# Kernel tuning notes

Measured on AMD Instinct MI355X. Metric: run time of the kernel, lower is better.

## Reference

```python
import jax, jax.numpy as jnp
import numpy as np

H = 16  # num_heads

def setup_inputs() -> dict:
    key = jax.random.key(0)
    ks = jax.random.split(key, 9)
    B, S, E = 2, 2048, 1024
    d = E // H  # 64, shared KV head dim
    sc = lambda n: 1.0 / np.sqrt(n)
    return {
        "x": jax.random.normal(ks[0], (B, S, E), jnp.float32),
        "wq": jax.random.normal(ks[1], (E, E), jnp.float32) * sc(E),
        "bq": jax.random.normal(ks[2], (E,), jnp.float32) * 0.02,
        "wk": jax.random.normal(ks[3], (E, d), jnp.float32) * sc(E),
        "bk": jax.random.normal(ks[4], (d,), jnp.float32) * 0.02,
        "wv": jax.random.normal(ks[5], (E, d), jnp.float32) * sc(E),
        "bv": jax.random.normal(ks[6], (d,), jnp.float32) * 0.02,
        "wo": jax.random.normal(ks[7], (E, E), jnp.float32) * sc(E),
        "bo": jax.random.normal(ks[8], (E,), jnp.float32) * 0.02,
    }

def reference(x, wq, bq, wk, bk, wv, bv, wo, bo):
    B, S, E = x.shape
    d = E // H
    Q = (x @ wq + bq).reshape(B, S, H, d).transpose(0, 2, 1, 3)  # [B,H,S,d]
    K = x @ wk + bk  # [B,S,d] shared across heads (MQA)
    V = x @ wv + bv  # [B,S,d]
    scores = jnp.einsum('bhqd,bkd->bhqk', Q, K) / np.sqrt(d)  # [B,H,S,S]
    weights = jax.nn.softmax(scores, axis=-1)
    attn = jnp.einsum('bhqk,bkd->bhqd', weights, V)  # [B,H,S,d]
    # FAITHFUL to source: reshape [B,H,S,d] -> [B,S,E] WITHOUT permuting back
    attn = attn.reshape(B, S, E)
    return attn @ wo + bo
```

## Files before the change

### kernel.cpp

```cpp
#include <hip/hip_runtime.h>
#include <hip/hip_bf16.h>

#define BB 2
#define SS 2048
#define EE 1024
#define HH 16
#define DD 64

using bfrag  = __attribute__((ext_vector_type(8))) short;
using bfrag4 = __attribute__((ext_vector_type(4))) short;
using ffrag  = __attribute__((ext_vector_type(4))) float;
using uint2v = __attribute__((ext_vector_type(2))) uint;

#define MFMA32(A, B, C) __builtin_amdgcn_mfma_f32_16x16x32_bf16(A, B, C, 0, 0, 0)
#define MFMA16(A, B, C) __builtin_amdgcn_mfma_f32_16x16x16bf16_1k(A, B, C, 0, 0, 0)

static __device__ __forceinline__ ushort f2bf(float f) {
  __hip_bfloat16 h = __float2bfloat16(f);
  return *reinterpret_cast<ushort*>(&h);
}

static __device__ __forceinline__ uint pack_bf2(float lo, float hi) {
  uint a = __float_as_uint(lo) + 0x8000u;
  uint b = __float_as_uint(hi) + 0x8000u;
  return __builtin_amdgcn_perm(b, a, 0x07060302u);
}

static __device__ __forceinline__ void gl_lds16(const ushort* g, ushort* l) {
  __builtin_amdgcn_global_load_lds(
      (const __attribute__((address_space(1))) void*)g,
      (__attribute__((address_space(3))) void*)l, 16, 0, 0);
}

__global__ __launch_bounds__(256) void prep(
    const float* __restrict__ x, const float* __restrict__ wq,
    const float* __restrict__ wk, const float* __restrict__ wv,
    const float* __restrict__ wo, ushort* __restrict__ xb,
    ushort* __restrict__ wqkvT, ushort* __restrict__ woT) {
  __shared__ float t[32][33];
  int id = blockIdx.x;
  if (id < 4096) {
    int i = id * 256 + threadIdx.x;
    float4 v = ((const float4*)x)[i];
    ushort4 u = { f2bf(v.x), f2bf(v.y), f2bf(v.z), f2bf(v.w) };
    ((ushort4*)xb)[i] = u;
    return;
  }
  id -= 4096;
  const float* src;
  ushort* dst;
  int N, bx, by;
  if (id < 1024)      { src = wq; dst = wqkvT;                      N = 1024; bx = id & 31;          by = id >> 5; }
  else if (id < 2048) { src = wo; dst = woT;                        N = 1024; bx = (id - 1024) & 31; by = (id - 1024) >> 5; }
  else if (id < 2112) { src = wk; dst = wqkvT + (size_t)1024 * 1024; N = 64;  bx = (id - 2048) & 1;  by = (id - 2048) >> 1; }
  else                { src = wv; dst = wqkvT + (size_t)1088 * 1024; N = 64;  bx = (id - 2112) & 1;  by = (id - 2112) >> 1; }
  const int k0 = by * 32, n0 = bx * 32;
  const int tx = threadIdx.x & 31, ty = threadIdx.x >> 5;
  #pragma unroll
  for (int i = 0; i < 32; i += 8)
    t[ty + i][tx] = src[(size_t)(k0 + ty + i) * N + n0 + tx];
  __syncthreads();
  #pragma unroll
  for (int i = 0; i < 32; i += 8)
    dst[(size_t)(n0 + ty + i) * 1024 + k0 + tx] = f2bf(t[tx][ty + i]);
}

template <bool QKV>
__global__ __launch_bounds__(256) void gemm_mfma3(
    const ushort* __restrict__ A, const ushort* __restrict__ Bt,
    const float* __restrict__ bias0, const float* __restrict__ bias1,
    const float* __restrict__ bias2, void* __restrict__ O1,
    ushort* __restrict__ Kb, ushort* __restrict__ VTb,
    int M, int N, int K, float qscale) {
  __shared__ __align__(16) ushort As[2][128 * 64];
  __shared__ __align__(16) ushort Bs[2][64 * 64];
  const int tid = threadIdx.x;
  const int lane = tid & 63;
  const int quad = lane >> 4;
  const int c = lane & 15;
  const int wv = tid >> 6;
  const int wm = (wv & 1) * 64;
  const int wn = (wv >> 1) * 32;
  const size_t m0 = (size_t)blockIdx.y * 128;
  const size_t n0 = (size_t)blockIdx.x * 64;

  const int srow = lane >> 3;
  const int sck = (lane & 7) ^ srow;

  ffrag zero = {0.f, 0.f, 0.f, 0.f};
  ffrag acc[4][2];
  #pragma unroll
  for (int mt = 0; mt < 4; ++mt)
    #pragma unroll
    for (int nt = 0; nt < 2; ++nt) acc[mt][nt] = zero;

  const int NK = K >> 6;
  #pragma unroll
  for (int i = 0; i < 4; ++i) {
    int ia = wv * 4 + i;
    gl_lds16(&A[(m0 + ia * 8 + srow) * (size_t)K + sck * 8], &As[0][ia * 512]);
  }
  #pragma unroll
  for (int i = 0; i < 2; ++i) {
    int ib = wv * 2 + i;
    gl_lds16(&Bt[(n0 + ib * 8 + srow) * (size_t)K + sck * 8], &Bs[0][ib * 512]);
  }
  __syncthreads();

  for (int ki = 0; ki < NK; ++ki) {
    const int buf = ki & 1;
    if (ki + 1 < NK) {
      int k0 = (ki + 1) << 6;
      #pragma unroll
      for (int i = 0; i < 4; ++i) {
        int ia = wv * 4 + i;
        gl_lds16(&A[(m0 + ia * 8 + srow) * (size_t)K + k0 + sck * 8],
                 &As[buf ^ 1][ia * 512]);
      }
      #pragma unroll
      for (int i = 0; i < 2; ++i) {
        int ib = wv * 2 + i;
        gl_lds16(&Bt[(n0 + ib * 8 + srow) * (size_t)K + k0 + sck * 8],
                 &Bs[buf ^ 1][ib * 512]);
      }
    }
    #pragma unroll
    for (int ks = 0; ks < 2; ++ks) {
      bfrag af[4], bf[2];
      #pragma unroll
      for (int mt = 0; mt < 4; ++mt) {
        int ra = wm + mt * 16 + c;
        af[mt] = *(const bfrag*)&As[buf][(ra * 8 + ((ks * 4 + quad) ^ (ra & 7))) * 8];
      }
      #pragma unroll
      for (int nt = 0; nt < 2; ++nt) {
        int rb = wn + nt * 16 + c;
        bf[nt] = *(const bfrag*)&Bs[buf][(rb * 8 + ((ks * 4 + quad) ^ (rb & 7))) * 8];
      }
      #pragma unroll
      for (int mt = 0; mt < 4; ++mt)
        #pragma unroll
        for (int nt = 0; nt < 2; ++nt)
          acc[mt][nt] = MFMA32(af[mt], bf[nt], acc[mt][nt]);
    }
    __syncthreads();
  }

  #pragma unroll
  for (int nt = 0; nt < 2; ++nt) {
    const int colb = (int)n0 + wn + nt * 16;
    if (QKV) {
      if (colb < 1024) {
        float bb = bias0[colb + c];
        ushort* dst = (ushort*)O1 + colb;
        #pragma unroll
        for (int mt = 0; mt < 4; ++mt)
          #pragma unroll
          for (int r = 0; r < 4; ++r) {
            size_t row = m0 + wm + mt * 16 + quad * 4 + r;
            dst[row * 1024 + c] = f2bf((acc[mt][nt][r] + bb) * qscale);
          }
      } else if (colb < 1088) {
        float bb = bias1[colb - 1024 + c];
        ushort* dst = Kb + (colb - 1024);
        #pragma unroll
        for (int mt = 0; mt < 4; ++mt)
          #pragma unroll
          for (int r = 0; r < 4; ++r) {
            size_t row = m0 + wm + mt * 16 + quad * 4 + r;
            dst[row * 64 + c] = f2bf(acc[mt][nt][r] + bb);
          }
      } else {
        int d = colb - 1088 + c;
        float bb = bias2[colb - 1088 + c];
        int bidx = (int)(m0 >> 11);
        ushort* dstv = VTb + ((size_t)(bidx * 64 + d)) * SS;
        #pragma unroll
        for (int mt = 0; mt < 4; ++mt) {
          int sb = (int)(m0 & 2047) + wm + mt * 16 + quad * 4;
          uint2v u;
          u.x = pack_bf2(acc[mt][nt][0] + bb, acc[mt][nt][1] + bb);
          u.y = pack_bf2(acc[mt][nt][2] + bb, acc[mt][nt][3] + bb);
          *(uint2v*)&dstv[sb] = u;
        }
      }
    } else {
      float bb = bias0[colb + c];
      float* dst = (float*)O1;
      #pragma unroll
      for (int mt = 0; mt < 4; ++mt)
        #pragma unroll
        for (int r = 0; r < 4; ++r) {
          size_t row = m0 + wm + mt * 16 + quad * 4 + r;
          dst[row * (size_t)N + colb + c] = acc[mt][nt][r] + bb;
        }
    }
  }
}

__global__ __launch_bounds__(256) void mqa_attn8(
    const ushort* __restrict__ Q, const ushort* __restrict__ Kg,
    const ushort* __restrict__ VT, ushort* __restrict__ A2) {
  __shared__ __align__(16) ushort Kt[2][4096];
  __shared__ __align__(16) ushort Vt[2][4096];
  const int tid = threadIdx.x;
  const int lane = tid & 63;
  const int quad = lane >> 4;
  const int c = lane & 15;
  const int wv = tid >> 6;
  const int bid = blockIdx.x;
  const int b = bid >> 8;
  const int r = bid & 255;
  const int h = r >> 4;
  const int s0 = (r & 15) << 7;

  const int srow = lane >> 3;
  const int sck = (lane & 7) ^ srow;

  ffrag zero = {0.f, 0.f, 0.f, 0.f};
  bfrag4 ones4;
  #pragma unroll
  for (int i = 0; i < 4; ++i) ones4[i] = (short)16256;

  bfrag aq[2][2];
  #pragma unroll
  for (int mt = 0; mt < 2; ++mt) {
    const ushort* qp =
        Q + ((size_t)(b * SS) + s0 + wv * 32 + mt * 16 + c) * EE + h * 64 + quad * 8;
    aq[mt][0] = *(const bfrag*)qp;
    aq[mt][1] = *(const bfrag*)(qp + 32);
  }

  ffrag o[2][4];
  #pragma unroll
  for (int mt = 0; mt < 2; ++mt)
    #pragma unroll
    for (int nt = 0; nt < 4; ++nt) o[mt][nt] = zero;
  ffrag ls[2] = {zero, zero};

  const ushort* Kbase = Kg + (size_t)b * SS * 64;
  const ushort* Vbase = VT + (size_t)b * 64 * SS;
  const int i0 = wv * 2, i1 = wv * 2 + 1;
  const int r0 = i0 * 8 + srow, r1 = i1 * 8 + srow;

  gl_lds16(Kbase + (size_t)r0 * 64 + sck * 8, &Kt[0][i0 * 512]);
  gl_lds16(Kbase + (size_t)r1 * 64 + sck * 8, &Kt[0][i1 * 512]);
  gl_lds16(Vbase + (size_t)r0 * SS + sck * 8, &Vt[0][i0 * 512]);
  gl_lds16(Vbase + (size_t)r1 * SS + sck * 8, &Vt[0][i1 * 512]);
  __syncthreads();

  for (int it = 0; it < 32; ++it) {
    const int buf = it & 1;
    if (it + 1 < 32) {
      int kb = (it + 1) << 6;
      gl_lds16(Kbase + (size_t)(kb + r0) * 64 + sck * 8, &Kt[buf ^ 1][i0 * 512]);
      gl_lds16(Kbase + (size_t)(kb + r1) * 64 + sck * 8, &Kt[buf ^ 1][i1 * 512]);
      gl_lds16(Vbase + (size_t)r0 * SS + kb + sck * 8, &Vt[buf ^ 1][i0 * 512]);
      gl_lds16(Vbase + (size_t)r1 * SS + kb + sck * 8, &Vt[buf ^ 1][i1 * 512]);
    }

    #pragma unroll
    for (int kt = 0; kt < 4; ++kt) {
      const int key = kt * 16 + c;
      const int k7 = key & 7;
      bfrag kf0 = *(const bfrag*)&Kt[buf][(key * 8 + (quad ^ k7)) * 8];
      bfrag kf1 = *(const bfrag*)&Kt[buf][(key * 8 + ((quad + 4) ^ k7)) * 8];
      bfrag4 pb[2];
      #pragma unroll
      for (int mt = 0; mt < 2; ++mt) {
        ffrag st = MFMA32(kf0, aq[mt][0], zero);
        st = MFMA32(kf1, aq[mt][1], st);
        uint2v uu;
        uu.x = pack_bf2(__builtin_amdgcn_exp2f(st[0]),
                        __builtin_amdgcn_exp2f(st[1]));
        uu.y = pack_bf2(__builtin_amdgcn_exp2f(st[2]),
                        __builtin_amdgcn_exp2f(st[3]));
        pb[mt] = __builtin_bit_cast(bfrag4, uu);
      }
      const int ck = kt * 2 + (quad >> 1);
      const int wc = (quad & 1) * 4;
      #pragma unroll
      for (int nt = 0; nt < 4; ++nt) {
        int d = nt * 16 + c;
        bfrag4 vf = *(const bfrag4*)&Vt[buf][(d * 8 + (ck ^ (d & 7))) * 8 + wc];
        #pragma unroll
        for (int mt = 0; mt < 2; ++mt)
          o[mt][nt] = MFMA16(vf, pb[mt], o[mt][nt]);
      }
      #pragma unroll
      for (int mt = 0; mt < 2; ++mt)
        ls[mt] = MFMA16(ones4, pb[mt], ls[mt]);
    }
    __syncthreads();
  }

  #pragma unroll
  for (int mt = 0; mt < 2; ++mt) {
    const float inv = 1.f / ls[mt][0];
    const int sp = h * 128 + (s0 >> 4) + wv * 2 + mt;
    ushort* orow = A2 + ((size_t)b * SS + sp) * EE;
    #pragma unroll
    for (int nt = 0; nt < 4; ++nt) {
      uint2v u;
      u.x = pack_bf2(o[mt][nt][0] * inv, o[mt][nt][1] * inv);
      u.y = pack_bf2(o[mt][nt][2] * inv, o[mt][nt][3] * inv);
      *(uint2v*)&orow[c * 64 + nt * 16 + quad * 4] = u;
    }
  }
}

extern "C" void kernel_launch(void* const* d_in, const int* in_sizes, int n_in,
                              void* d_out, int out_size, void* d_ws, size_t ws_size,
                              hipStream_t stream) {
  const float* x  = (const float*)d_in[0];
  const float* wq = (const float*)d_in[1];
  const float* bq = (const float*)d_in[2];
  const float* wk = (const float*)d_in[3];
  const float* bk = (const float*)d_in[4];
  const float* wv = (const float*)d_in[5];
  const float* bv = (const float*)d_in[6];
  const float* wo = (const float*)d_in[7];
  const float* bo = (const float*)d_in[8];
  float* out = (float*)d_out;

  char* w = (char*)d_ws;
  ushort* xb     = (ushort*)w;  w += (size_t)4096 * 1024 * 2;
  ushort* wqkvT  = (ushort*)w;  w += (size_t)1152 * 1024 * 2;
  ushort* woT    = (ushort*)w;  w += (size_t)1024 * 1024 * 2;
  ushort* Qb     = (ushort*)w;  w += (size_t)4096 * 1024 * 2;
  ushort* Kb     = (ushort*)w;  w += (size_t)4096 * 64 * 2;
  ushort* VTb    = (ushort*)w;  w += (size_t)BB * 64 * SS * 2;
  ushort* A2     = (ushort*)w;  w += (size_t)4096 * 1024 * 2;

  prep<<<6272, 256, 0, stream>>>(x, wq, wk, wv, wo, xb, wqkvT, woT);

  const float qscale = 0.18033688011112042f;
  gemm_mfma3<true><<<dim3(18, 32), 256, 0, stream>>>(
      xb, wqkvT, bq, bk, bv, Qb, Kb, VTb, 4096, 1152, 1024, qscale);

  mqa_attn8<<<512, 256, 0, stream>>>(Qb, Kb, VTb, A2);

  gemm_mfma3<false><<<dim3(16, 32), 256, 0, stream>>>(
      A2, woT, bo, nullptr, nullptr, out, nullptr, nullptr, 4096, 1024, 1024, 1.0f);
}
```

Baseline: 186.5 us.

## Split attention key range across two wave groups and merge partials in LDS

```diff
diff --git a/kernel.cpp b/kernel.cpp
--- a/kernel.cpp
+++ b/kernel.cpp
@@ -198,16 +198,18 @@
   }
 }
 
-__global__ __launch_bounds__(256) void mqa_attn8(
+__global__ __launch_bounds__(512) void mqa_attn10(
     const ushort* __restrict__ Q, const ushort* __restrict__ Kg,
     const ushort* __restrict__ VT, ushort* __restrict__ A2) {
-  __shared__ __align__(16) ushort Kt[2][4096];
-  __shared__ __align__(16) ushort Vt[2][4096];
+  __shared__ __align__(16) ushort Kt[2][2][4096];
+  __shared__ __align__(16) ushort Vt[2][2][4096];
   const int tid = threadIdx.x;
   const int lane = tid & 63;
   const int quad = lane >> 4;
   const int c = lane & 15;
   const int wv = tid >> 6;
+  const int half = wv >> 2;
+  const int lw = wv & 3;
   const int bid = blockIdx.x;
   const int b = bid >> 8;
   const int r = bid & 255;
@@ -226,7 +228,7 @@
   #pragma unroll
   for (int mt = 0; mt < 2; ++mt) {
     const ushort* qp =
-        Q + ((size_t)(b * SS) + s0 + wv * 32 + mt * 16 + c) * EE + h * 64 + quad * 8;
+        Q + ((size_t)(b * SS) + s0 + lw * 32 + mt * 16 + c) * EE + h * 64 + quad * 8;
     aq[mt][0] = *(const bfrag*)qp;
     aq[mt][1] = *(const bfrag*)(qp + 32);
   }
@@ -238,33 +240,34 @@
     for (int nt = 0; nt < 4; ++nt) o[mt][nt] = zero;
   ffrag ls[2] = {zero, zero};
 
+  const int koff = half << 10;
   const ushort* Kbase = Kg + (size_t)b * SS * 64;
   const ushort* Vbase = VT + (size_t)b * 64 * SS;
-  const int i0 = wv * 2, i1 = wv * 2 + 1;
+  const int i0 = lw * 2, i1 = lw * 2 + 1;
   const int r0 = i0 * 8 + srow, r1 = i1 * 8 + srow;
 
-  gl_lds16(Kbase + (size_t)r0 * 64 + sck * 8, &Kt[0][i0 * 512]);
-  gl_lds16(Kbase + (size_t)r1 * 64 + sck * 8, &Kt[0][i1 * 512]);
-  gl_lds16(Vbase + (size_t)r0 * SS + sck * 8, &Vt[0][i0 * 512]);
-  gl_lds16(Vbase + (size_t)r1 * SS + sck * 8, &Vt[0][i1 * 512]);
+  gl_lds16(Kbase + (size_t)(koff + r0) * 64 + sck * 8, &Kt[half][0][i0 * 512]);
+  gl_lds16(Kbase + (size_t)(koff + r1) * 64 + sck * 8, &Kt[half][0][i1 * 512]);
+  gl_lds16(Vbase + (size_t)r0 * SS + koff + sck * 8, &Vt[half][0][i0 * 512]);
+  gl_lds16(Vbase + (size_t)r1 * SS + koff + sck * 8, &Vt[half][0][i1 * 512]);
   __syncthreads();
 
-  for (int it = 0; it < 32; ++it) {
+  for (int it = 0; it < 16; ++it) {
     const int buf = it & 1;
-    if (it + 1 < 32) {
-      int kb = (it + 1) << 6;
-      gl_lds16(Kbase + (size_t)(kb + r0) * 64 + sck * 8, &Kt[buf ^ 1][i0 * 512]);
-      gl_lds16(Kbase + (size_t)(kb + r1) * 64 + sck * 8, &Kt[buf ^ 1][i1 * 512]);
-      gl_lds16(Vbase + (size_t)r0 * SS + kb + sck * 8, &Vt[buf ^ 1][i0 * 512]);
-      gl_lds16(Vbase + (size_t)r1 * SS + kb + sck * 8, &Vt[buf ^ 1][i1 * 512]);
+    if (it + 1 < 16) {
+      int kb = koff + ((it + 1) << 6);
+      gl_lds16(Kbase + (size_t)(kb + r0) * 64 + sck * 8, &Kt[half][buf ^ 1][i0 * 512]);
+      gl_lds16(Kbase + (size_t)(kb + r1) * 64 + sck * 8, &Kt[half][buf ^ 1][i1 * 512]);
+      gl_lds16(Vbase + (size_t)r0 * SS + kb + sck * 8, &Vt[half][buf ^ 1][i0 * 512]);
+      gl_lds16(Vbase + (size_t)r1 * SS + kb + sck * 8, &Vt[half][buf ^ 1][i1 * 512]);
     }
 
     #pragma unroll
     for (int kt = 0; kt < 4; ++kt) {
       const int key = kt * 16 + c;
       const int k7 = key & 7;
-      bfrag kf0 = *(const bfrag*)&Kt[buf][(key * 8 + (quad ^ k7)) * 8];
-      bfrag kf1 = *(const bfrag*)&Kt[buf][(key * 8 + ((quad + 4) ^ k7)) * 8];
+      bfrag kf0 = *(const bfrag*)&Kt[half][buf][(key * 8 + (quad ^ k7)) * 8];
+      bfrag kf1 = *(const bfrag*)&Kt[half][buf][(key * 8 + ((quad + 4) ^ k7)) * 8];
       bfrag4 pb[2];
       #pragma unroll
       for (int mt = 0; mt < 2; ++mt) {
@@ -282,7 +285,7 @@
       #pragma unroll
       for (int nt = 0; nt < 4; ++nt) {
         int d = nt * 16 + c;
-        bfrag4 vf = *(const bfrag4*)&Vt[buf][(d * 8 + (ck ^ (d & 7))) * 8 + wc];
+        bfrag4 vf = *(const bfrag4*)&Vt[half][buf][(d * 8 + (ck ^ (d & 7))) * 8 + wc];
         #pragma unroll
         for (int mt = 0; mt < 2; ++mt)
           o[mt][nt] = MFMA16(vf, pb[mt], o[mt][nt]);
@@ -294,10 +297,31 @@
     __syncthreads();
   }
 
+  float* cbuf = (float*)&Kt[0][0][0];
+  float* lbuf = (float*)&Vt[0][0][0];
+  if (half == 1) {
+    float* wb = cbuf + (size_t)lw * 2048;
+    #pragma unroll
+    for (int mt = 0; mt < 2; ++mt) {
+      #pragma unroll
+      for (int nt = 0; nt < 4; ++nt)
+        *(ffrag*)&wb[(mt * 4 + nt) * 256 + lane * 4] = o[mt][nt];
+      lbuf[lw * 128 + mt * 64 + lane] = ls[mt][0];
+    }
+  }
+  __syncthreads();
+  if (half == 1) return;
+
+  const float* rb = cbuf + (size_t)lw * 2048;
   #pragma unroll
   for (int mt = 0; mt < 2; ++mt) {
-    const float inv = 1.f / ls[mt][0];
-    const int sp = h * 128 + (s0 >> 4) + wv * 2 + mt;
+    #pragma unroll
+    for (int nt = 0; nt < 4; ++nt) {
+      ffrag p = *(const ffrag*)&rb[(mt * 4 + nt) * 256 + lane * 4];
+      o[mt][nt] += p;
+    }
+    const float inv = 1.f / (ls[mt][0] + lbuf[lw * 128 + mt * 64 + lane]);
+    const int sp = h * 128 + (s0 >> 4) + lw * 2 + mt;
     ushort* orow = A2 + ((size_t)b * SS + sp) * EE;
     #pragma unroll
     for (int nt = 0; nt < 4; ++nt) {
@@ -338,7 +362,7 @@
   gemm_mfma3<true><<<dim3(18, 32), 256, 0, stream>>>(
       xb, wqkvT, bq, bk, bv, Qb, Kb, VTb, 4096, 1152, 1024, qscale);
 
-  mqa_attn8<<<512, 256, 0, stream>>>(Qb, Kb, VTb, A2);
+  mqa_attn10<<<512, 512, 0, stream>>>(Qb, Kb, VTb, A2);
 
   gemm_mfma3<false><<<dim3(16, 32), 256, 0, stream>>>(
       A2, woT, bo, nullptr, nullptr, out, nullptr, nullptr, 4096, 1024, 1024, 1.0f);
```

Measured after the change: 169.8 us. 1.1x faster.
